# Optimization experiments

Measured on AMD Instinct MI355X. Metric: run time of the kernel, lower is better.

Reference implementation:

```python
import jax, jax.numpy as jnp
import numpy as np

# Module hyperparameters (init_kwargs)
RADIUS = 0.3
NSAMPLE = 64
NORMALIZE_XYZ = True

B, N, M, C = 8, 20000, 1024, 128  # batch, points, centers, feature channels


def setup_inputs() -> dict:
    key = jax.random.key(0)
    k1, k2, k3, k4, k5 = jax.random.split(key, 5)
    # points uniform in a side-2 cube -> each radius-0.3 ball holds ~280 pts
    xyz = jax.random.uniform(k1, (B, N, 3), jnp.float32) * 2.0
    new_xyz = jax.random.uniform(k2, (B, M, 3), jnp.float32) * 2.0
    batch_distances = jax.random.uniform(k3, (B, M), jnp.float32)
    inds = jax.random.randint(k4, (B, M), 0, N, jnp.int64)
    features = jax.random.normal(k5, (B, C, N), jnp.float32)
    return {"xyz": xyz, "new_xyz": new_xyz, "batch_distances": batch_distances,
            "inds": inds, "features": features}


def ball_query(xyz, new_xyz):
    """Standard pointnet2 ball query: first NSAMPLE indices with d^2 < r^2,
    remaining slots filled with the first in-range index. -> (B, M, NSAMPLE) int32."""
    n = xyz.shape[1]
    # (B, M, N) squared distances
    d2 = jnp.sum((new_xyz[:, :, None, :] - xyz[:, None, :, :]) ** 2, axis=-1)
    mask = d2 < (RADIUS * RADIUS)
    ar = jnp.arange(n, dtype=jnp.int32)
    # sort key: valid indices keep their index (in order), invalid pushed to back
    sort_key = jnp.where(mask, ar, ar + n)
    order = jnp.argsort(sort_key, axis=-1)[..., :NSAMPLE].astype(jnp.int32)
    cnt = jnp.sum(mask, axis=-1)  # (B, M) number of in-range points
    slot = jnp.arange(NSAMPLE, dtype=cnt.dtype)
    # slots beyond cnt are filled with the first valid index (0 if cnt == 0)
    idx = jnp.where(slot[None, None, :] < jnp.maximum(cnt, 1)[..., None],
                    order, order[..., :1])
    return idx


def reference(xyz, new_xyz, batch_distances, inds, features):
    # batch_distances / inds only accelerate the original cpp kernel; the math
    # is the plain radius search below.
    idx = ball_query(xyz, new_xyz)  # (B, M, S)
    # group xyz: (B, M, S, 3) -> (B, 3, M, S)
    grouped_xyz = jax.vmap(lambda pts, i: pts[i])(xyz, idx)
    grouped_xyz = jnp.transpose(grouped_xyz, (0, 3, 1, 2))
    grouped_xyz = grouped_xyz - jnp.transpose(new_xyz, (0, 2, 1))[..., None]
    if NORMALIZE_XYZ:
        grouped_xyz = grouped_xyz / RADIUS
    # group features: (B, C, M, S)
    grouped_features = jax.vmap(lambda f, i: f[:, i])(features, idx)
    new_features = jnp.concatenate([grouped_xyz, grouped_features], axis=1)
    return (new_features, idx)
```

## Files before the change

### kernel.cpp

```cpp
#include <hip/hip_runtime.h>

#define B_ 8
#define N_ 20000
#define M_ 1024
#define C_ 128
#define S_ 64
#define NCH_ 131
#define CHUNK_ 2048
#define NCHK_ ((N_ + CHUNK_ - 1) / CHUNK_)

typedef float  vf4 __attribute__((ext_vector_type(4)));

__global__ __launch_bounds__(256) void query_kernel(
    const float* __restrict__ xyz,
    const float* __restrict__ new_xyz,
    float* __restrict__ out,
    int* __restrict__ iws)
{
    const int tid  = threadIdx.x;
    const int wid  = tid >> 6;
    const int lane = tid & 63;
    const int bm   = blockIdx.x;
    const int b    = bm >> 10;
    const int m    = bm & (M_ - 1);

    __shared__ int s_idx[S_];
    __shared__ int s_tot[2][4];

    const float cx = new_xyz[bm * 3 + 0];
    const float cy = new_xyz[bm * 3 + 1];
    const float cz = new_xyz[bm * 3 + 2];
    const float r2 = (float)(0.3 * 0.3);
    const float* xb = xyz + (size_t)b * N_ * 3;
    const unsigned long long below = (1ull << lane) - 1ull;

#define LOAD_TILE(F, INB, NB, CB) do {                                        \
    NB = (CB) + (wid << 9) + (lane << 3);                                     \
    INB = (NB < N_);        \
    if (INB) {                                                                \
        const float4* p4_ = (const float4*)(xb + (size_t)NB * 3);             \
        _Pragma("unroll")                                                     \
        for (int q = 0; q < 6; ++q) {                                         \
            const float4 v_ = p4_[q];                                         \
            F[4*q+0] = v_.x; F[4*q+1] = v_.y; F[4*q+2] = v_.z; F[4*q+3] = v_.w; \
        }                                                                     \
    } } while (0)

#define PROC_TILE(F, INB, NB, PAR) do {                                       \
    unsigned vbits = 0;                                                       \
    if (INB) {                                                                \
        _Pragma("unroll")                                                     \
        for (int j = 0; j < 8; ++j) {                                         \
            const float dx = __fadd_rn(F[3*j+0], -cx);                        \
            const float dy = __fadd_rn(F[3*j+1], -cy);                        \
            const float dz = __fadd_rn(F[3*j+2], -cz);                        \
            const float d2 = __fadd_rn(                                       \
                __fadd_rn(__fmul_rn(dx, dx), __fmul_rn(dy, dy)),              \
                __fmul_rn(dz, dz));                                           \
            if (d2 < r2) vbits |= (1u << j);                                  \
        }                                                                     \
    }                                                                         \
    int pre = 0, tot = 0;                                                     \
    _Pragma("unroll")                                                         \
    for (int j = 0; j < 8; ++j) {                                             \
        const unsigned long long mk = __ballot((vbits >> j) & 1u);            \
        pre += __popcll(mk & below);                                          \
        tot += __popcll(mk);                                                  \
    }                                                                         \
    if (lane == 0) s_tot[PAR][wid] = tot;                                     \
    __syncthreads();                                                          \
    int off = cnt;                                                            \
    _Pragma("unroll")                                                         \
    for (int w = 0; w < 4; ++w) { if (w < wid) off += s_tot[PAR][w]; }        \
    int pos = off + pre;                                                      \
    _Pragma("unroll")                                                         \
    for (int j = 0; j < 8; ++j) {                                             \
        if (vbits & (1u << j)) {                                              \
            if (pos < S_) s_idx[pos] = NB + j;                                \
            ++pos;                                                            \
        }                                                                     \
    }                                                                         \
    cnt += s_tot[PAR][0] + s_tot[PAR][1] + s_tot[PAR][2] + s_tot[PAR][3];     \
    } while (0)

#define STAGE(PF, PINB, PNB, RF, RINB, RNB, PAR) do {                         \
    if (t_load < NCHK_) { LOAD_TILE(RF, RINB, RNB, t_load * CHUNK_); }        \
    ++t_load;                                                                 \
    PROC_TILE(PF, PINB, PNB, PAR);                                            \
    ++t_proc;                                                                 \
    if (cnt >= S_ || t_proc >= NCHK_) goto qdone;                             \
    } while (0)

    int cnt = 0;
    float fA[24], fB[24];
    bool inbA = false, inbB = false;
    int nA = 0, nB = 0;

    LOAD_TILE(fA, inbA, nA, 0);
    int t_load = 1, t_proc = 0;

    for (;;) {
        STAGE(fA, inbA, nA, fB, inbB, nB, 0);
        STAGE(fB, inbB, nB, fA, inbA, nA, 1);
    }
qdone:
#undef LOAD_TILE
#undef PROC_TILE
#undef STAGE

    __syncthreads();
    {
        const int c = cnt < S_ ? cnt : S_;
        const int first = (c > 0) ? s_idx[0] : 0;
        if (tid >= c && tid < S_) s_idx[tid] = first;
    }
    __syncthreads();

    if (tid < S_) {
        const int n = s_idx[tid];
        float* out_idx = out + (size_t)B_ * NCH_ * M_ * S_;
        __builtin_nontemporal_store((float)n, &out_idx[(size_t)bm * S_ + tid]);
        iws[(size_t)bm * S_ + tid] = n;
    }
    if (tid < 3 * S_) {
        const int ch = tid >> 6;
        const int s  = tid & 63;
        const int n  = s_idx[s];
        const float cc = new_xyz[bm * 3 + ch];
        const float v = (xb[n * 3 + ch] - cc) / 0.3f;
        __builtin_nontemporal_store(v,
            &out[(((size_t)b * NCH_ + ch) * M_ + m) * S_ + s]);
    }
}

__global__ __launch_bounds__(256) void group_feat_kernel(
    const float* __restrict__ features,
    const int* __restrict__ iws,
    float* __restrict__ out)
{
    const int b  = blockIdx.x & 7;
    const int ch = blockIdx.x >> 3;

    __shared__ float slice[N_];

    const float* fb = features + ((size_t)b * C_ + ch) * N_;
    const vf4* fb4 = (const vf4*)fb;
    vf4* sl4 = (vf4*)slice;
    for (int i = threadIdx.x; i < N_ / 4; i += 256)
        sl4[i] = __builtin_nontemporal_load(&fb4[i]);
    __syncthreads();

    const int* ib = iws + (size_t)b * M_ * S_;
    float* ob = out + ((size_t)b * NCH_ + 3 + ch) * (size_t)(M_ * S_);
    for (int e = threadIdx.x * 4; e < M_ * S_; e += 256 * 4) {
        const int4 ii = *(const int4*)(ib + e);
        vf4 w;
        w.x = slice[ii.x]; w.y = slice[ii.y];
        w.z = slice[ii.z]; w.w = slice[ii.w];
        __builtin_nontemporal_store(w, (vf4*)(ob + e));
    }
}

__global__ __launch_bounds__(256) void qg_fused(
    const float* __restrict__ xyz,
    const float* __restrict__ new_xyz,
    const float* __restrict__ features,
    float* __restrict__ out)
{
    const int bm = blockIdx.x;
    const int b  = bm >> 10;
    const int m  = bm & (M_ - 1);
    const int tid = threadIdx.x;

    __shared__ int s_idx[S_];

    if (tid < 64) {
        const int lane = tid;
        const float cx = new_xyz[bm * 3 + 0];
        const float cy = new_xyz[bm * 3 + 1];
        const float cz = new_xyz[bm * 3 + 2];
        const float r2 = (float)(0.3 * 0.3);
        const float* xb = xyz + (size_t)b * N_ * 3;

        int cnt = 0;
        for (int base = 0; base < N_; base += 64) {
            const int n = base + lane;
            bool valid = false;
            if (n < N_) {
                const float dx = __fadd_rn(xb[n * 3 + 0], -cx);
                const float dy = __fadd_rn(xb[n * 3 + 1], -cy);
                const float dz = __fadd_rn(xb[n * 3 + 2], -cz);
                const float d2 = __fadd_rn(
                    __fadd_rn(__fmul_rn(dx, dx), __fmul_rn(dy, dy)),
                    __fmul_rn(dz, dz));
                valid = d2 < r2;
            }
            const unsigned long long mk = __ballot(valid);
            if (valid) {
                const int pos = cnt + __popcll(mk & ((1ull << lane) - 1ull));
                if (pos < S_) s_idx[pos] = n;
            }
            cnt += __popcll(mk);
            if (cnt >= S_) break;
        }
        const int c = cnt < S_ ? cnt : S_;
        const int first = (c > 0) ? s_idx[0] : 0;
        if (lane >= c) s_idx[lane] = first;

        float* out_idx = out + (size_t)B_ * NCH_ * M_ * S_;
        out_idx[(size_t)bm * S_ + lane] = (float)s_idx[lane];
    }
    __syncthreads();

    if (tid < 3 * S_) {
        const int ch = tid >> 6;
        const int s  = tid & 63;
        const int n  = s_idx[s];
        const float v = (xyz[((size_t)b * N_ + n) * 3 + ch] - new_xyz[bm * 3 + ch]) / 0.3f;
        out[(((size_t)b * NCH_ + ch) * M_ + m) * S_ + s] = v;
    }

    const int s  = tid & 63;
    const int cq = tid >> 6;
    const int n  = s_idx[s];
    const float* fb = features + (size_t)b * C_ * N_;
    float* ob = out + (((size_t)b * NCH_ + 3) * M_ + m) * S_ + s;
    for (int ch = cq; ch < C_; ch += 4) {
        ob[(size_t)ch * (M_ * S_)] = fb[(size_t)ch * N_ + n];
    }
}

extern "C" void kernel_launch(void* const* d_in, const int* in_sizes, int n_in,
                              void* d_out, int out_size, void* d_ws, size_t ws_size,
                              hipStream_t stream) {
    const float* xyz      = (const float*)d_in[0];
    const float* new_xyz  = (const float*)d_in[1];
    const float* features = (const float*)d_in[4];
    float* out = (float*)d_out;

    const size_t need = (size_t)B_ * M_ * S_ * sizeof(int);
    if (ws_size < need) {
        qg_fused<<<B_ * M_, 256, 0, stream>>>(xyz, new_xyz, features, out);
        return;
    }
    int* iws = (int*)d_ws;

    query_kernel<<<B_ * M_, 256, 0, stream>>>(xyz, new_xyz, out, iws);
    group_feat_kernel<<<B_ * C_, 256, 0, stream>>>(features, iws, out);
}
```

Measured before the change: 131.2 us.

## Stage xyz chunks through LDS with coalesced loads and smaller chunks

The ball-query loop now copies each chunk of point coordinates into a double-buffered shared-memory tile using fully coalesced float4 loads, instead of each thread loading 8 consecutive points into registers. Points are then mapped lane-interleaved, and the prefix scan is done with per-j ballots. The chunk size drops from 2048 to 1024, so the early exit after 64 hits wastes fewer scanned points. In exchange the kernel uses 24 KB of LDS per block, which may limit occupancy, and adds a block-wide copy stage per chunk.

```diff
diff --git a/kernel.cpp b/kernel.cpp
--- a/kernel.cpp
+++ b/kernel.cpp
@@ -6,8 +6,10 @@
 #define C_ 128
 #define S_ 64
 #define NCH_ 131
-#define CHUNK_ 2048
+#define CHUNK_ 1024
 #define NCHK_ ((N_ + CHUNK_ - 1) / CHUNK_)
+#define CF4_ ((CHUNK_ * 3) / 4)
+#define XYZF4MAX_ ((B_ * N_ * 3) / 4 - 1)
 
 typedef float  vf4 __attribute__((ext_vector_type(4)));
 
@@ -24,6 +26,7 @@
     const int b    = bm >> 10;
     const int m    = bm & (M_ - 1);
 
+    __shared__ __align__(16) float s_pts[2][CHUNK_ * 3];
     __shared__ int s_idx[S_];
     __shared__ int s_tot[2][4];
 
@@ -31,82 +34,77 @@
     const float cy = new_xyz[bm * 3 + 1];
     const float cz = new_xyz[bm * 3 + 2];
     const float r2 = (float)(0.3 * 0.3);
-    const float* xb = xyz + (size_t)b * N_ * 3;
     const unsigned long long below = (1ull << lane) - 1ull;
 
-#define LOAD_TILE(F, INB, NB, CB) do {                                        \
-    NB = (CB) + (wid << 9) + (lane << 3);                                     \
-    INB = (NB < N_);        \
-    if (INB) {                                                                \
-        const float4* p4_ = (const float4*)(xb + (size_t)NB * 3);             \
+    const float4* g4 = (const float4*)xyz;
+    const int batch_f4 = b * ((N_ * 3) / 4);
+
+#define STAGE_CHUNK(T, DST) do {                                              \
+        const int cb4 = batch_f4 + (T) * CF4_;                                \
+        float4* d4 = (float4*)(DST);                                          \
         _Pragma("unroll")                                                     \
-        for (int q = 0; q < 6; ++q) {                                         \
-            const float4 v_ = p4_[q];                                         \
-            F[4*q+0] = v_.x; F[4*q+1] = v_.y; F[4*q+2] = v_.z; F[4*q+3] = v_.w; \
+        for (int k = 0; k < CF4_ / 256; ++k) {                                \
+            int gi = cb4 + k * 256 + tid;                                     \
+            gi = gi < XYZF4MAX_ ? gi : XYZF4MAX_;    \
+            d4[k * 256 + tid] = g4[gi];                                       \
         }                                                                     \
-    } } while (0)
-
-#define PROC_TILE(F, INB, NB, PAR) do {                                       \
-    unsigned vbits = 0;                                                       \
-    if (INB) {                                                                \
-        _Pragma("unroll")                                                     \
-        for (int j = 0; j < 8; ++j) {                                         \
-            const float dx = __fadd_rn(F[3*j+0], -cx);                        \
-            const float dy = __fadd_rn(F[3*j+1], -cy);                        \
-            const float dz = __fadd_rn(F[3*j+2], -cz);                        \
-            const float d2 = __fadd_rn(                                       \
-                __fadd_rn(__fmul_rn(dx, dx), __fmul_rn(dy, dy)),              \
-                __fmul_rn(dz, dz));                                           \
-            if (d2 < r2) vbits |= (1u << j);                                  \
-        }                                                                     \
-    }                                                                         \
-    int pre = 0, tot = 0;                                                     \
-    _Pragma("unroll")                                                         \
-    for (int j = 0; j < 8; ++j) {                                             \
-        const unsigned long long mk = __ballot((vbits >> j) & 1u);            \
-        pre += __popcll(mk & below);                                          \
-        tot += __popcll(mk);                                                  \
-    }                                                                         \
-    if (lane == 0) s_tot[PAR][wid] = tot;                                     \
-    __syncthreads();                                                          \
-    int off = cnt;                                                            \
-    _Pragma("unroll")                                                         \
-    for (int w = 0; w < 4; ++w) { if (w < wid) off += s_tot[PAR][w]; }        \
-    int pos = off + pre;                                                      \
-    _Pragma("unroll")                                                         \
-    for (int j = 0; j < 8; ++j) {                                             \
-        if (vbits & (1u << j)) {                                              \
-            if (pos < S_) s_idx[pos] = NB + j;                                \
-            ++pos;                                                            \
-        }                                                                     \
-    }                                                                         \
-    cnt += s_tot[PAR][0] + s_tot[PAR][1] + s_tot[PAR][2] + s_tot[PAR][3];     \
     } while (0)
 
-#define STAGE(PF, PINB, PNB, RF, RINB, RNB, PAR) do {                         \
-    if (t_load < NCHK_) { LOAD_TILE(RF, RINB, RNB, t_load * CHUNK_); }        \
-    ++t_load;                                                                 \
-    PROC_TILE(PF, PINB, PNB, PAR);                                            \
-    ++t_proc;                                                                 \
-    if (cnt >= S_ || t_proc >= NCHK_) goto qdone;                             \
-    } while (0)
-
     int cnt = 0;
-    float fA[24], fB[24];
-    bool inbA = false, inbB = false;
-    int nA = 0, nB = 0;
-
-    LOAD_TILE(fA, inbA, nA, 0);
-    int t_load = 1, t_proc = 0;
+    int t = 0, par = 0;
+
+    STAGE_CHUNK(0, s_pts[0]);
+    __syncthreads();
 
     for (;;) {
-        STAGE(fA, inbA, nA, fB, inbB, nB, 0);
-        STAGE(fB, inbB, nB, fA, inbA, nA, 1);
-    }
-qdone:
-#undef LOAD_TILE
-#undef PROC_TILE
-#undef STAGE
+        const float* cur = s_pts[par];
+        if (t + 1 < NCHK_) STAGE_CHUNK(t + 1, s_pts[par ^ 1]);
+
+        unsigned vbits = 0;
+        int tot = 0;
+#pragma unroll
+        for (int j = 0; j < 4; ++j) {
+            const int pl = (wid << 8) + (j << 6) + lane;
+            const int n  = t * CHUNK_ + pl;
+            bool valid = false;
+            if (n < N_) {
+                const float* pp = cur + 3 * pl;
+                const float dx = __fadd_rn(pp[0], -cx);
+                const float dy = __fadd_rn(pp[1], -cy);
+                const float dz = __fadd_rn(pp[2], -cz);
+                const float d2 = __fadd_rn(
+                    __fadd_rn(__fmul_rn(dx, dx), __fmul_rn(dy, dy)),
+                    __fmul_rn(dz, dz));
+                valid = d2 < r2;
+            }
+            const unsigned long long mk = __ballot(valid);
+            if (valid) vbits |= (1u << j);
+            tot += __popcll(mk);
+        }
+        if (lane == 0) s_tot[par][wid] = tot;
+        __syncthreads();
+
+        int off = cnt;
+#pragma unroll
+        for (int w = 0; w < 4; ++w) { if (w < wid) off += s_tot[par][w]; }
+
+        int jbase = off;
+#pragma unroll
+        for (int j = 0; j < 4; ++j) {
+            const unsigned long long mk = __ballot((vbits >> j) & 1u);
+            if ((vbits >> j) & 1u) {
+                const int pos = jbase + __popcll(mk & below);
+                if (pos < S_) s_idx[pos] = t * CHUNK_ + (wid << 8) + (j << 6) + lane;
+            }
+            jbase += __popcll(mk);
+        }
+        cnt += s_tot[par][0] + s_tot[par][1] + s_tot[par][2] + s_tot[par][3];
+
+        ++t;
+        par ^= 1;
+        if (cnt >= S_ || t >= NCHK_) break;
+    }
+#undef STAGE_CHUNK
 
     __syncthreads();
     {
@@ -116,6 +114,7 @@
     }
     __syncthreads();
 
+    const float* xb = xyz + (size_t)b * N_ * 3;
     if (tid < S_) {
         const int n = s_idx[tid];
         float* out_idx = out + (size_t)B_ * NCH_ * M_ * S_;
```

After: 146.8 us. +11.9%, slower.
